# Optimization experiments

Hardware: AMD Instinct MI355X
Metric: run time of the kernel (lower is better)

Reference implementation:

```python
import jax, jax.numpy as jnp
import numpy as np

TAU = 2.0       # LIF membrane time constant
V_TH = 1.0      # spike threshold
ALPHA = 2.0     # ATan surrogate sharpness
EPS = 1e-5      # BatchNorm eps


@jax.custom_vjp
def spike_fn(x):
    return (x >= 0.0).astype(x.dtype)

def _spike_fwd(x):
    return spike_fn(x), x

def _spike_bwd(x, g):
    # ATan surrogate: alpha/2 / (1 + (pi/2 * alpha * x)^2)
    sg = (ALPHA / 2.0) / (1.0 + (jnp.pi / 2.0 * ALPHA * x) ** 2)
    return (g * sg,)

spike_fn.defvjp(_spike_fwd, _spike_bwd)


def lif_multistep(x):
    # x: [T, B, C, L]; spikingjelly LIFNode, decay_input=True, hard reset to 0,
    # detach_reset=True (spike detached in the reset path only).
    def step(v, xt):
        v = v + (xt - v) / TAU
        s = spike_fn(v - V_TH)
        v = (1.0 - jax.lax.stop_gradient(s)) * v
        return v, s
    v0 = jnp.zeros_like(x[0])
    _, spks = jax.lax.scan(step, v0, x)
    return spks  # [T, B, C, L]


def delta_encoder(inputs, bn_gamma, bn_beta, enc_w, enc_b):
    # inputs: [B, L, C]
    delta = jnp.concatenate(
        [jnp.zeros_like(inputs[:, :1]), inputs[:, 1:] - inputs[:, :-1]], axis=1
    )  # [B, L, C]
    d = jnp.transpose(delta, (0, 2, 1))[:, None]  # [B, 1, C, L]
    # BatchNorm2d(1), training mode: stats over all elements (single channel)
    mean = jnp.mean(d)
    var = jnp.var(d)
    d = (d - mean) * jax.lax.rsqrt(var + EPS) * bn_gamma[0] + bn_beta[0]
    d = jnp.transpose(d, (0, 2, 3, 1))  # [B, C, L, 1]
    # Linear(1, T): enc[b,c,l,t] = d[b,c,l,0] * w[t,0] + b[t]
    enc = d * enc_w[:, 0] + enc_b  # [B, C, L, T]
    enc = jnp.transpose(enc, (3, 0, 1, 2))  # [T, B, C, L]
    spks = lif_multistep(enc)
    return jnp.transpose(spks, (1, 0, 2, 3))  # [B, T, C, L]


def setup_inputs() -> dict:
    key = jax.random.key(0)
    k1, k2, k3 = jax.random.split(key, 3)
    B, L, C, T = 32, 4096, 8, 64
    inputs = jax.random.normal(k1, (B, L, C), dtype=jnp.float32)
    bn_gamma = jnp.ones((1,), dtype=jnp.float32)
    bn_beta = jnp.zeros((1,), dtype=jnp.float32)
    # torch Linear(1, T) init: U(-1, 1) since fan_in = 1
    enc_w = jax.random.uniform(k2, (T, 1), dtype=jnp.float32, minval=-1.0, maxval=1.0)
    enc_b = jax.random.uniform(k3, (T,), dtype=jnp.float32, minval=-1.0, maxval=1.0)
    return {"inputs": inputs, "bn_gamma": bn_gamma, "bn_beta": bn_beta,
            "enc_w": enc_w, "enc_b": enc_b}


def reference(inputs, bn_gamma, bn_beta, enc_w, enc_b):
    return delta_encoder(inputs, bn_gamma, bn_beta, enc_w, enc_b)
```

## Files before the change

### kernel.cpp

```cpp
#include <hip/hip_runtime.h>
#include <math.h>

#define NBATCH 32
#define NL     4096
#define NC     8
#define NT     64
#define NTOT   (NBATCH * NL * NC)

typedef float f32x4 __attribute__((ext_vector_type(4)));

__global__ __launch_bounds__(256) void reduce_kernel(const float* __restrict__ in,
                                                     double* __restrict__ part) {
    __shared__ double sm[256], sm2[256];
    const int tid = threadIdx.x;
    const f32x4* in4 = reinterpret_cast<const f32x4*>(in);
    double s = 0.0, s2 = 0.0;
    for (int g = blockIdx.x * 256 + tid; g < NTOT / 4; g += 256 * 256) {
        const int e = g * 4;
        if ((e & (NL * NC - 1)) >= NC) {
            const f32x4 cur = in4[g];
            const f32x4 prv = in4[g - 2];
            const double d0 = (double)cur.x - (double)prv.x;
            const double d1 = (double)cur.y - (double)prv.y;
            const double d2 = (double)cur.z - (double)prv.z;
            const double d3 = (double)cur.w - (double)prv.w;
            s  += d0 + d1 + d2 + d3;
            s2 += d0 * d0 + d1 * d1 + d2 * d2 + d3 * d3;
        }
    }
    sm[tid] = s; sm2[tid] = s2;
    __syncthreads();
    for (int off = 128; off > 0; off >>= 1) {
        if (tid < off) { sm[tid] += sm[tid + off]; sm2[tid] += sm2[tid + off]; }
        __syncthreads();
    }
    if (tid == 0) {
        part[2 * blockIdx.x]     = sm[0];
        part[2 * blockIdx.x + 1] = sm2[0];
    }
}

__global__ __launch_bounds__(256) void finalize_kernel(const double* __restrict__ part,
                                                       const float* __restrict__ gamma,
                                                       const float* __restrict__ beta,
                                                       const float* __restrict__ wv,
                                                       const float* __restrict__ bv,
                                                       double2* __restrict__ pq) {
    __shared__ double sm[256], sm2[256];
    __shared__ double sAB[2];
    const int tid = threadIdx.x;
    sm[tid]  = part[2 * tid];
    sm2[tid] = part[2 * tid + 1];
    __syncthreads();
    for (int off = 128; off > 0; off >>= 1) {
        if (tid < off) { sm[tid] += sm[tid + off]; sm2[tid] += sm2[tid + off]; }
        __syncthreads();
    }
    if (tid == 0) {
        const double mean = sm[0] / (double)NTOT;
        const double var  = sm2[0] / (double)NTOT - mean * mean;
        const double inv  = 1.0 / sqrt(var + 1e-5);
        const double A    = inv * (double)gamma[0];
        const double Bc   = (double)beta[0] - mean * A;
        sAB[0] = A;
        sAB[1] = Bc;
    }
    __syncthreads();
    if (tid < NT) {
        const double A  = sAB[0];
        const double Bc = sAB[1];
        const double w  = (double)wv[tid];
        const double b  = (double)bv[tid];
        double2 r;
        r.x = 0.5 * A * w;
        r.y = 0.5 * (Bc * w + b);
        pq[tid] = r;
    }
}

__global__ __launch_bounds__(512) void lif_kernel(const float* __restrict__ in,
                                                  const double2* __restrict__ pq,
                                                  float* __restrict__ out) {
    __shared__ __align__(16) double2 spq[NT];
    const int tid = threadIdx.x;
    if (tid < NT) spq[tid] = pq[tid];
    __syncthreads();

    const int blk  = blockIdx.x;
    const int half = blk & 1;
    const int c    = (blk >> 1) & 7;
    const int b    = blk >> 4;
    const int l    = half * 2048 + tid * 4;

    const float* base = in + (b * NL + l) * NC + c;
    const float xm = (l == 0) ? 0.0f : base[-NC];
    const float x0 = base[0];
    const float x1 = base[NC];
    const float x2 = base[2 * NC];
    const float x3 = base[3 * NC];

    const double d0 = (l == 0) ? 0.0 : ((double)x0 - (double)xm);
    const double d1 = (double)x1 - (double)x0;
    const double d2 = (double)x2 - (double)x1;
    const double d3 = (double)x3 - (double)x2;

    double v0 = 0.0, v1 = 0.0, v2 = 0.0, v3 = 0.0;

    float4* op = reinterpret_cast<float4*>(out + ((b * NT) * NC + c) * NL + l);
    const int tstride = NC * NL / 4;

    unsigned mA0 = 0, mA1 = 0, mA2 = 0, mA3 = 0;
#pragma unroll 8
    for (int t = 0; t < 32; ++t) {
        const double2 PQ = spq[t];
        double vv; bool s;
        vv = fma(v0, 0.5, fma(d0, PQ.x, PQ.y)); s = vv >= 1.0; mA0 = mA0 + mA0 + (s ? 1u : 0u); v0 = s ? 0.0 : vv;
        vv = fma(v1, 0.5, fma(d1, PQ.x, PQ.y)); s = vv >= 1.0; mA1 = mA1 + mA1 + (s ? 1u : 0u); v1 = s ? 0.0 : vv;
        vv = fma(v2, 0.5, fma(d2, PQ.x, PQ.y)); s = vv >= 1.0; mA2 = mA2 + mA2 + (s ? 1u : 0u); v2 = s ? 0.0 : vv;
        vv = fma(v3, 0.5, fma(d3, PQ.x, PQ.y)); s = vv >= 1.0; mA3 = mA3 + mA3 + (s ? 1u : 0u); v3 = s ? 0.0 : vv;
    }

#pragma unroll 8
    for (int t = 0; t < 32; ++t) {
        float4 o;
        o.x = ((int)mA0 < 0) ? 1.0f : 0.0f; mA0 <<= 1;
        o.y = ((int)mA1 < 0) ? 1.0f : 0.0f; mA1 <<= 1;
        o.z = ((int)mA2 < 0) ? 1.0f : 0.0f; mA2 <<= 1;
        o.w = ((int)mA3 < 0) ? 1.0f : 0.0f; mA3 <<= 1;
        op[t * tstride] = o;
    }

    unsigned mB0 = 0, mB1 = 0, mB2 = 0, mB3 = 0;
#pragma unroll 8
    for (int t = 32; t < 64; ++t) {
        const double2 PQ = spq[t];
        double vv; bool s;
        vv = fma(v0, 0.5, fma(d0, PQ.x, PQ.y)); s = vv >= 1.0; mB0 = mB0 + mB0 + (s ? 1u : 0u); v0 = s ? 0.0 : vv;
        vv = fma(v1, 0.5, fma(d1, PQ.x, PQ.y)); s = vv >= 1.0; mB1 = mB1 + mB1 + (s ? 1u : 0u); v1 = s ? 0.0 : vv;
        vv = fma(v2, 0.5, fma(d2, PQ.x, PQ.y)); s = vv >= 1.0; mB2 = mB2 + mB2 + (s ? 1u : 0u); v2 = s ? 0.0 : vv;
        vv = fma(v3, 0.5, fma(d3, PQ.x, PQ.y)); s = vv >= 1.0; mB3 = mB3 + mB3 + (s ? 1u : 0u); v3 = s ? 0.0 : vv;
    }

#pragma unroll 8
    for (int t = 32; t < 64; ++t) {
        float4 o;
        o.x = ((int)mB0 < 0) ? 1.0f : 0.0f; mB0 <<= 1;
        o.y = ((int)mB1 < 0) ? 1.0f : 0.0f; mB1 <<= 1;
        o.z = ((int)mB2 < 0) ? 1.0f : 0.0f; mB2 <<= 1;
        o.w = ((int)mB3 < 0) ? 1.0f : 0.0f; mB3 <<= 1;
        op[t * tstride] = o;
    }
}

extern "C" void kernel_launch(void* const* d_in, const int* in_sizes, int n_in,
                              void* d_out, int out_size, void* d_ws, size_t ws_size,
                              hipStream_t stream) {
    const float* inputs = (const float*)d_in[0];
    const float* gamma  = (const float*)d_in[1];
    const float* beta   = (const float*)d_in[2];
    const float* enc_w  = (const float*)d_in[3];
    const float* enc_b  = (const float*)d_in[4];
    float* out = (float*)d_out;

    double*  part = (double*)d_ws;
    double2* pq   = (double2*)(part + 512);

    reduce_kernel  <<<256, 256, 0, stream>>>(inputs, part);
    finalize_kernel<<<1,   256, 0, stream>>>(part, gamma, beta, enc_w, enc_b, pq);
    lif_kernel     <<<512, 512, 0, stream>>>(inputs, pq, out);
}
```

Baseline: 281.0 us.

## Split LIF into bitmask compute kernel and fully-parallel expand kernel

The LIF kernel now packs spike bits into 64-bit-per-element masks in workspace rather than writing the float output directly. A new expand kernel then reads the masks and writes the float output with many more blocks and a linear, fully coalesced store pattern. The goal is to lift the low occupancy of the 512-block LIF kernel during its large 256 MB output write. The cost is an extra launch and an extra round trip through workspace (about 8 MB of masks).

```diff
diff --git a/kernel.cpp b/kernel.cpp
--- a/kernel.cpp
+++ b/kernel.cpp
@@ -6,6 +6,7 @@
 #define NC     8
 #define NT     64
 #define NTOT   (NBATCH * NL * NC)
+#define MASK4_HALF (NTOT / 4)
 
 typedef float f32x4 __attribute__((ext_vector_type(4)));
 
@@ -78,9 +79,9 @@
     }
 }
 
-__global__ __launch_bounds__(512) void lif_kernel(const float* __restrict__ in,
-                                                  const double2* __restrict__ pq,
-                                                  float* __restrict__ out) {
+__global__ __launch_bounds__(512) void lif_mask_kernel(const float* __restrict__ in,
+                                                       const double2* __restrict__ pq,
+                                                       uint4* __restrict__ msk) {
     __shared__ __align__(16) double2 spq[NT];
     const int tid = threadIdx.x;
     if (tid < NT) spq[tid] = pq[tid];
@@ -106,9 +107,6 @@
 
     double v0 = 0.0, v1 = 0.0, v2 = 0.0, v3 = 0.0;
 
-    float4* op = reinterpret_cast<float4*>(out + ((b * NT) * NC + c) * NL + l);
-    const int tstride = NC * NL / 4;
-
     unsigned mA0 = 0, mA1 = 0, mA2 = 0, mA3 = 0;
 #pragma unroll 8
     for (int t = 0; t < 32; ++t) {
@@ -119,17 +117,6 @@
         vv = fma(v2, 0.5, fma(d2, PQ.x, PQ.y)); s = vv >= 1.0; mA2 = mA2 + mA2 + (s ? 1u : 0u); v2 = s ? 0.0 : vv;
         vv = fma(v3, 0.5, fma(d3, PQ.x, PQ.y)); s = vv >= 1.0; mA3 = mA3 + mA3 + (s ? 1u : 0u); v3 = s ? 0.0 : vv;
     }
-
-#pragma unroll 8
-    for (int t = 0; t < 32; ++t) {
-        float4 o;
-        o.x = ((int)mA0 < 0) ? 1.0f : 0.0f; mA0 <<= 1;
-        o.y = ((int)mA1 < 0) ? 1.0f : 0.0f; mA1 <<= 1;
-        o.z = ((int)mA2 < 0) ? 1.0f : 0.0f; mA2 <<= 1;
-        o.w = ((int)mA3 < 0) ? 1.0f : 0.0f; mA3 <<= 1;
-        op[t * tstride] = o;
-    }
-
     unsigned mB0 = 0, mB1 = 0, mB2 = 0, mB3 = 0;
 #pragma unroll 8
     for (int t = 32; t < 64; ++t) {
@@ -141,14 +128,30 @@
         vv = fma(v3, 0.5, fma(d3, PQ.x, PQ.y)); s = vv >= 1.0; mB3 = mB3 + mB3 + (s ? 1u : 0u); v3 = s ? 0.0 : vv;
     }
 
+    const int idx = b * 8192 + c * 1024 + (l >> 2);
+    uint4 a; a.x = mA0; a.y = mA1; a.z = mA2; a.w = mA3;
+    uint4 bb; bb.x = mB0; bb.y = mB1; bb.z = mB2; bb.w = mB3;
+    msk[idx]              = a;
+    msk[idx + MASK4_HALF] = bb;
+}
+
+__global__ __launch_bounds__(256) void expand_kernel(const uint4* __restrict__ msk,
+                                                     float4* __restrict__ out) {
+    int g = blockIdx.x * 256 + threadIdx.x;
 #pragma unroll 8
-    for (int t = 32; t < 64; ++t) {
+    for (int k = 0; k < 32; ++k, g += 2048 * 256) {
+        const int slab = g >> 13;
+        const int j4   = g & 8191;
+        const int t    = slab & 63;
+        const int b    = slab >> 6;
+        const uint4 m  = msk[(t >> 5) * MASK4_HALF + b * 8192 + j4];
+        const int sh   = t & 31;
         float4 o;
-        o.x = ((int)mB0 < 0) ? 1.0f : 0.0f; mB0 <<= 1;
-        o.y = ((int)mB1 < 0) ? 1.0f : 0.0f; mB1 <<= 1;
-        o.z = ((int)mB2 < 0) ? 1.0f : 0.0f; mB2 <<= 1;
-        o.w = ((int)mB3 < 0) ? 1.0f : 0.0f; mB3 <<= 1;
-        op[t * tstride] = o;
+        o.x = __uint_as_float(((unsigned)((int)(m.x << sh) >> 31)) & 0x3F800000u);
+        o.y = __uint_as_float(((unsigned)((int)(m.y << sh) >> 31)) & 0x3F800000u);
+        o.z = __uint_as_float(((unsigned)((int)(m.z << sh) >> 31)) & 0x3F800000u);
+        o.w = __uint_as_float(((unsigned)((int)(m.w << sh) >> 31)) & 0x3F800000u);
+        out[g] = o;
     }
 }
 
@@ -164,8 +167,10 @@
 
     double*  part = (double*)d_ws;
     double2* pq   = (double2*)(part + 512);
+    uint4*   msk  = (uint4*)((char*)d_ws + 8192);
 
-    reduce_kernel  <<<256, 256, 0, stream>>>(inputs, part);
-    finalize_kernel<<<1,   256, 0, stream>>>(part, gamma, beta, enc_w, enc_b, pq);
-    lif_kernel     <<<512, 512, 0, stream>>>(inputs, pq, out);
+    reduce_kernel  <<<256,  256, 0, stream>>>(inputs, part);
+    finalize_kernel<<<1,    256, 0, stream>>>(part, gamma, beta, enc_w, enc_b, pq);
+    lif_mask_kernel<<<512,  512, 0, stream>>>(inputs, pq, msk);
+    expand_kernel  <<<2048, 256, 0, stream>>>(msk, (float4*)out);
 }
```

After: 306.5 us. 9.1% more time.
